# Kernel tuning notes

Measured on AMD Instinct MI355X. Metric: run time of the kernel, lower is better.

## Reference

```python
import jax, jax.numpy as jnp
import numpy as np

SCALES = [1, 2, 4]
DM = 768          # d_model
DS = 256          # d_scale = d_model / num_scales
DI = 512          # d_inner = expand * d_scale
N = 16            # d_state
K = 4             # d_conv (mamba causal conv)
R = 16            # dt_rank = ceil(d_scale/16)
B = 8
L = 1024
BN_EPS = 1e-5


def setup_inputs() -> dict:
    key = jax.random.key(0)
    ks = iter(jax.random.split(key, 64))
    def rn(shape, s=0.02):
        return jax.random.normal(next(ks), shape, jnp.float32) * s
    lengths = jax.random.randint(next(ks), (B,), L // 2, L + 1)
    mask = (jnp.arange(L)[None, :] < lengths[:, None]).astype(jnp.int32)
    return {
        "hidden_input": jax.random.normal(next(ks), (B, L, DM), jnp.float32),
        "mask": mask,
        # per-scale depthwise dilated conv + BN (eval-mode stats)
        "pool_w": rn((3, DS, 1, 3), 0.2),
        "pool_b": rn((3, DS)),
        "bn_g": jnp.ones((3, DS), jnp.float32),
        "bn_b": jnp.zeros((3, DS), jnp.float32),
        "bn_rm": jnp.zeros((3, DS), jnp.float32),
        "bn_rv": jnp.ones((3, DS), jnp.float32),
        # mamba params, axes = [scale(3), direction(2: fwd/bwd), ...]
        "in_proj_w": rn((3, 2, 2 * DI, DS)),
        "conv_w": rn((3, 2, DI, 1, K), 0.2),
        "conv_b": rn((3, 2, DI)),
        "x_proj_w": rn((3, 2, R + 2 * N, DI)),
        "dt_w": rn((3, 2, DI, R), 0.1),
        "dt_b": rn((3, 2, DI), 0.1),
        "A_log": jnp.broadcast_to(
            jnp.log(jnp.arange(1, N + 1, dtype=jnp.float32)), (3, 2, DI, N)
        ),
        "Dp": jnp.ones((3, 2, DI), jnp.float32),
        "mo_w": rn((3, 2, DS, DI)),
        # ExBimamba output_proj (2*d_scale -> d_scale, with bias)
        "op_w": rn((3, DS, 2 * DS)),
        "op_b": rn((3, DS)),
        # channel attention MLP (no bias) and fusion linear
        "ca_w1": rn((DM // 2, DM)),
        "ca_w2": rn((DM, DM // 2)),
        "fus_w": rn((DM, DM)),
        "fus_b": rn((DM,)),
    }


def _causal_dw_conv(x, w, b):
    # x: [B,L,D], w: [D,1,K] -> causal depthwise conv (left pad K-1)
    y = jax.lax.conv_general_dilated(
        x.transpose(0, 2, 1), w, (1,), [(K - 1, 0)],
        feature_group_count=w.shape[0], dimension_numbers=("NCH", "OIH", "NCH"))
    return y.transpose(0, 2, 1) + b


def _dilated_same_conv(x, w, b, dil):
    # x: [B,C,L], w: [C,1,3], depthwise, padding='same' with dilation
    y = jax.lax.conv_general_dilated(
        x, w, (1,), "SAME", rhs_dilation=(dil,),
        feature_group_count=x.shape[1], dimension_numbers=("NCH", "OIH", "NCH"))
    return y + b[:, None]


def _selective_scan(x, dt, A, Bm, Cm):
    # x, dt: [B,L,DI]; A: [DI,N]; Bm, Cm: [B,L,N]
    def step(h, inp):
        xt, dtt, Bt, Ct = inp
        h = h * jnp.exp(dtt[..., None] * A) + (dtt * xt)[..., None] * Bt[:, None, :]
        return h, jnp.einsum("bdn,bn->bd", h, Ct)
    h0 = jnp.zeros((x.shape[0], x.shape[2], A.shape[1]), x.dtype)
    _, ys = jax.lax.scan(
        step, h0,
        (x.swapaxes(0, 1), dt.swapaxes(0, 1), Bm.swapaxes(0, 1), Cm.swapaxes(0, 1)))
    return ys.swapaxes(0, 1)


def _mamba(u, iw, cw, cb, xw, dw, db, alog, D, ow):
    # u: [B,L,DS] -> [B,L,DS]
    x, z = jnp.split(u @ iw.T, 2, axis=-1)          # each [B,L,DI]
    x = jax.nn.silu(_causal_dw_conv(x, cw, cb))
    xdbl = x @ xw.T                                  # [B,L,R+2N]
    dt = jax.nn.softplus(xdbl[..., :R] @ dw.T + db)  # [B,L,DI]
    Bm, Cm = xdbl[..., R:R + N], xdbl[..., R + N:]
    y = _selective_scan(x, dt, -jnp.exp(alog), Bm, Cm) + x * D
    return (y * jax.nn.silu(z)) @ ow.T


def _mask_flip(x, lengths):
    # reverse the valid prefix of each row, keep padding in place (involution)
    j = jnp.arange(x.shape[1])
    idx = jnp.where(j[None, :] < lengths[:, None],
                    lengths[:, None] - 1 - j[None, :], j[None, :])
    return jnp.take_along_axis(x, idx[:, :, None], axis=1)


def reference(hidden_input, mask, pool_w, pool_b, bn_g, bn_b, bn_rm, bn_rv,
              in_proj_w, conv_w, conv_b, x_proj_w, dt_w, dt_b, A_log, Dp,
              mo_w, op_w, op_b, ca_w1, ca_w2, fus_w, fus_b):
    lengths = mask.sum(1)
    xs = jnp.split(hidden_input, 3, axis=-1)
    outs = []
    for i, s in enumerate(SCALES):
        c = _dilated_same_conv(xs[i].transpose(0, 2, 1), pool_w[i], pool_b[i], s)
        c = (c - bn_rm[i][:, None]) / jnp.sqrt(bn_rv[i][:, None] + BN_EPS) \
            * bn_g[i][:, None] + bn_b[i][:, None]
        c = jax.nn.gelu(c, approximate=False).transpose(0, 2, 1)  # [B,L,DS]
        f = _mamba(c, in_proj_w[i, 0], conv_w[i, 0], conv_b[i, 0], x_proj_w[i, 0],
                   dt_w[i, 0], dt_b[i, 0], A_log[i, 0], Dp[i, 0], mo_w[i, 0])
        bi = _mask_flip(c, lengths)
        bwd = _mamba(bi, in_proj_w[i, 1], conv_w[i, 1], conv_b[i, 1], x_proj_w[i, 1],
                     dt_w[i, 1], dt_b[i, 1], A_log[i, 1], Dp[i, 1], mo_w[i, 1])
        bwd = _mask_flip(bwd, lengths)
        outs.append(jnp.concatenate([f, bwd], -1) @ op_w[i].T + op_b[i])
    out = jnp.concatenate(outs, -1)                 # [B,L,DM]
    # channel attention: pools over the sequence (length) axis
    avg, mx = out.mean(1), out.max(1)
    def mlp(v):
        return jax.nn.relu(v @ ca_w1.T) @ ca_w2.T
    att = jax.nn.sigmoid(mlp(avg) + mlp(mx))
    out = out * att[:, None, :]
    return out @ fus_w.T + fus_b                    # dropout: eval-mode identity
```

## Files before the change

kernel.cpp:

```cpp
#include <hip/hip_runtime.h>
#include <cstddef>
#include <cstdint>

#define LQ 1024
#define DMQ 768
#define DSQ 256
#define DIQ 512
#define CCH 8
#define CT (LQ / CCH)

typedef unsigned short ushortT;
using f32x4 = __attribute__((ext_vector_type(4))) float;
using bf16x8 = __attribute__((ext_vector_type(8))) short;
using u16x8 = __attribute__((ext_vector_type(8))) unsigned short;

__device__ __forceinline__ float sigf(float x) { return 1.f / (1.f + __expf(-x)); }
__device__ __forceinline__ float softplusf(float x) {
    return fmaxf(x, 0.f) + __logf(1.f + __expf(-fabsf(x)));
}
__device__ __forceinline__ ushortT f2bf(float f) {
    unsigned u = __float_as_uint(f);
    u += 0x7FFFu + ((u >> 16) & 1u);
    return (ushortT)(u >> 16);
}
__device__ __forceinline__ float bf2f(ushortT u) {
    return __uint_as_float(((unsigned)u) << 16);
}
__device__ __forceinline__ void gload_lds16(const void* g, void* l) {
    __builtin_amdgcn_global_load_lds((const __attribute__((address_space(1))) void*)g,
                                     (__attribute__((address_space(3))) void*)l, 16, 0, 0);
}

__global__ void k_lengths(const int* __restrict__ mask, int* __restrict__ lengths) {
    int b = blockIdx.x;
    int s = 0;
    for (int t = threadIdx.x; t < LQ; t += 256) s += mask[b * LQ + t];
    __shared__ int sm[256];
    sm[threadIdx.x] = s;
    __syncthreads();
    for (int o = 128; o > 0; o >>= 1) {
        if (threadIdx.x < o) sm[threadIdx.x] += sm[threadIdx.x + o];
        __syncthreads();
    }
    if (threadIdx.x == 0) lengths[b] = sm[0];
}

__global__ void k_prep(const float* __restrict__ ipw, const float* __restrict__ fusw,
                       const float* __restrict__ xpw, ushortT* __restrict__ ipwb,
                       ushortT* __restrict__ fuswb, ushortT* __restrict__ xpwb) {
    int i = blockIdx.x * 256 + threadIdx.x;
    if (i < 1572864) { ipwb[i] = f2bf(ipw[i]); return; }
    i -= 1572864;
    if (i < 589824) { fuswb[i] = f2bf(fusw[i]); return; }
    i -= 589824;
    if (i >= 393216) return;
    int inst = i >> 16, rem = i & 65535;
    int row = rem >> 9, col = rem & 511;
    float v = (row < 48) ? xpw[((size_t)inst * 48 + row) * 512 + col] : 0.f;
    xpwb[i] = f2bf(v);
}

__global__ void k_wfuse(const float* __restrict__ opw, const float* __restrict__ mow,
                        ushortT* __restrict__ wf) {
    int idx = blockIdx.x * 256 + threadIdx.x;
    int inst = idx >> 15;
    int rem = idx & 32767;
    int m = rem >> 7;
    int d0 = (rem & 127) * 4;
    int i = inst >> 1, dir = inst & 1;
    const float* a = opw + (size_t)i * 131072 + dir * 256 + (size_t)m * 512;
    const float* bm = mow + (size_t)inst * 131072 + d0;
    float s0 = 0.f, s1 = 0.f, s2 = 0.f, s3 = 0.f;
    for (int c = 0; c < 256; c++) {
        float av = a[c];
        float4 bv = *(const float4*)(bm + (size_t)c * 512);
        s0 = fmaf(av, bv.x, s0);
        s1 = fmaf(av, bv.y, s1);
        s2 = fmaf(av, bv.z, s2);
        s3 = fmaf(av, bv.w, s3);
    }
    ushort4 r = {f2bf(s0), f2bf(s1), f2bf(s2), f2bf(s3)};
    *(ushort4*)(wf + ((size_t)i * 256 + m) * 1024 + dir * 512 + d0) = r;
}

__global__ void k_fusw8(const float* __restrict__ fusw, const float* __restrict__ att,
                        ushortT* __restrict__ wf8) {
    int idx = blockIdx.x * 256 + threadIdx.x;
    int b = idx / 147456;
    int rem = idx % 147456;
    int n = rem / 192;
    int k0 = (rem % 192) * 4;
    float4 w = *(const float4*)(fusw + (size_t)n * 768 + k0);
    float4 a = *(const float4*)(att + (size_t)b * 768 + k0);
    ushort4 r = {f2bf(w.x * a.x), f2bf(w.y * a.y), f2bf(w.z * a.z), f2bf(w.w * a.w)};
    *(ushort4*)(wf8 + ((size_t)(b * 768 + n)) * 768 + k0) = r;
}

__global__ __launch_bounds__(64) void k_pool(const float* __restrict__ hid,
                                             const float* __restrict__ pw,
                                             const float* __restrict__ pb,
                                             const float* __restrict__ bg,
                                             const float* __restrict__ bb,
                                             const float* __restrict__ brm,
                                             const float* __restrict__ brv,
                                             ushortT* __restrict__ cdst) {
    int gidx = blockIdx.x;
    int isc = gidx >> 13;
    int idx = gidx & 8191;
    int l = idx & (LQ - 1);
    int b = idx >> 10;
    int ch0 = threadIdx.x * 4;
    int dil = 1 << isc;
    int wci0 = isc * DSQ + ch0;
    const float* xb = hid + (size_t)b * LQ * DMQ + isc * DSQ + ch0;
    float wv[12];
    *(float4*)&wv[0] = *(const float4*)(pw + (size_t)wci0 * 3);
    *(float4*)&wv[4] = *(const float4*)(pw + (size_t)wci0 * 3 + 4);
    *(float4*)&wv[8] = *(const float4*)(pw + (size_t)wci0 * 3 + 8);
    float pbv[4], bgv[4], bbv[4], rmv[4], rvv[4];
    *(float4*)pbv = *(const float4*)(pb + wci0);
    *(float4*)bgv = *(const float4*)(bg + wci0);
    *(float4*)bbv = *(const float4*)(bb + wci0);
    *(float4*)rmv = *(const float4*)(brm + wci0);
    *(float4*)rvv = *(const float4*)(brv + wci0);
    float xm[4] = {0.f, 0.f, 0.f, 0.f}, xc[4], xp[4] = {0.f, 0.f, 0.f, 0.f};
    int lm = l - dil, lp = l + dil;
    if (lm >= 0) *(float4*)xm = *(const float4*)(xb + (size_t)lm * DMQ);
    *(float4*)xc = *(const float4*)(xb + (size_t)l * DMQ);
    if (lp < LQ) *(float4*)xp = *(const float4*)(xb + (size_t)lp * DMQ);
    ushort4 o;
#pragma unroll
    for (int j = 0; j < 4; j++) {
        float acc = pbv[j];
        acc = fmaf(wv[j * 3 + 0], xm[j], acc);
        acc = fmaf(wv[j * 3 + 1], xc[j], acc);
        acc = fmaf(wv[j * 3 + 2], xp[j], acc);
        float xn = (acc - rmv[j]) * rsqrtf(rvv[j] + 1e-5f) * bgv[j] + bbv[j];
        float y = 0.5f * xn * (1.0f + erff(xn * 0.70710678118654752f));
        ((ushortT*)&o)[j] = f2bf(y);
    }
    *(ushort4*)(cdst + (size_t)isc * 2097152 + (size_t)idx * DSQ + ch0) = o;
}

template <int FLIPA, int FLIPC, int BIAS, int ACC, int CBF16, int GATE>
__global__ __launch_bounds__(256) void gemm_bf16(
    const ushortT* __restrict__ A, const ushortT* __restrict__ Bw, void* __restrict__ Cv,
    const float* __restrict__ bias, const ushortT* __restrict__ Yb,
    const int* __restrict__ lengths, int N, int Kd, int lda, int ldc, int ldy, long sAz,
    int zshiftA, long sBz, long sCz, long sCzOdd, int zshiftC, long sYz, int sBiasz) {
    __shared__ ushortT Als[128 * 64];
    __shared__ ushortT Bls[128 * 64];
    const int z = blockIdx.z;
    A += (size_t)(z >> zshiftA) * sAz;
    Bw += (size_t)z * sBz;
    size_t cbase = (size_t)(z >> zshiftC) * sCz +
                   (size_t)(z & ((1 << zshiftC) - 1)) * sCzOdd;
    float* Cf = (float*)Cv + (CBF16 ? 0 : cbase);
    ushortT* Cb = (ushortT*)Cv + (CBF16 ? cbase : 0);
    if (BIAS) bias += (size_t)z * sBiasz;
    if (GATE) Yb += (size_t)z * sYz;

    const int tid = threadIdx.x;
    const int lane = tid & 63;
    const int wave = tid >> 6;
    const int wr = wave >> 1, wc = wave & 1;
    const int row0 = blockIdx.y * 128, col0 = blockIdx.x * 128;
    const bool doflipA = (FLIPA == 1) || (FLIPA == 2 && (z & 1));
    const bool doflipC = (FLIPC == 1) || (FLIPC == 2 && (z & 1));
    int len = 0;
    if (FLIPA || FLIPC) len = lengths[row0 >> 10];

    const int srow = wave * 8 + (lane >> 3);
    const int scol = (lane & 7) * 8;

    f32x4 acc[4][4];
#pragma unroll
    for (int i = 0; i < 4; i++)
#pragma unroll
        for (int j = 0; j < 4; j++) acc[i][j] = (f32x4){0.f, 0.f, 0.f, 0.f};

    for (int k0 = 0; k0 < Kd; k0 += 64) {
        __syncthreads();
#pragma unroll
        for (int it = 0; it < 4; it++) {
            int row = it * 32 + srow;
            int grow = row0 + row;
            if (FLIPA) {
                if (doflipA) {
                    int t = grow & (LQ - 1);
                    int ts = (t < len) ? (len - 1 - t) : t;
                    grow = (grow & ~(LQ - 1)) | ts;
                }
            }
            gload_lds16(A + (size_t)grow * lda + k0 + scol, &Als[it * 2048 + wave * 512]);
        }
#pragma unroll
        for (int it = 0; it < 4; it++) {
            int row = it * 32 + srow;
            gload_lds16(Bw + (size_t)(col0 + row) * Kd + k0 + scol,
                        &Bls[it * 2048 + wave * 512]);
        }
        __syncthreads();
#pragma unroll
        for (int ks = 0; ks < 2; ks++) {
            bf16x8 am[4], bv[4];
#pragma unroll
            for (int f = 0; f < 4; f++) {
                am[f] = *(const bf16x8*)&Als[(wr * 64 + f * 16 + (lane & 15)) * 64 + ks * 32 +
                                             (lane >> 4) * 8];
                bv[f] = *(const bf16x8*)&Bls[(wc * 64 + f * 16 + (lane & 15)) * 64 + ks * 32 +
                                             (lane >> 4) * 8];
            }
#pragma unroll
            for (int fm = 0; fm < 4; fm++)
#pragma unroll
                for (int fn = 0; fn < 4; fn++)
                    acc[fm][fn] = __builtin_amdgcn_mfma_f32_16x16x32_bf16(am[fm], bv[fn],
                                                                          acc[fm][fn], 0, 0, 0);
        }
    }
#pragma unroll
    for (int fm = 0; fm < 4; fm++) {
#pragma unroll
        for (int r = 0; r < 4; r++) {
            int growY = row0 + wr * 64 + fm * 16 + (lane >> 4) * 4 + r;
            int growC = growY;
            if (FLIPC) {
                if (doflipC) {
                    int t = growC & (LQ - 1);
                    int ts = (t < len) ? (len - 1 - t) : t;
                    growC = (growC & ~(LQ - 1)) | ts;
                }
            }
#pragma unroll
            for (int fn = 0; fn < 4; fn++) {
                int col = col0 + wc * 64 + fn * 16 + (lane & 15);
                if (col < N) {
                    float v = acc[fm][fn][r];
                    if (CBF16) {
                        if (GATE) {
                            float yv = bf2f(Yb[(size_t)growY * ldy + col]);
                            v = yv * v * sigf(v);
                        }
                        if (BIAS) v += bias[col];
                        Cb[(size_t)growC * ldc + col] = f2bf(v);
                    } else {
                        float* cp = Cf + (size_t)growC * ldc + col;
                        if (ACC) v += *cp;
                        if (BIAS) v += bias[col];
                        *cp = v;
                    }
                }
            }
        }
    }
}

__global__ __launch_bounds__(256) void k_dwconv(const ushortT* __restrict__ rawx,
                                                const float* __restrict__ cw,
                                                const float* __restrict__ cb,
                                                ushortT* __restrict__ sx) {
    int blk = blockIdx.x;
    int tc = blk & 7;
    int sb = blk >> 3;
    int inst = sb >> 3;
    int cg = threadIdx.x & 63;
    int sub = threadIdx.x >> 6;
    int ch0 = cg * 8;
    int t0 = tc * 128 + sub * 32;
    const ushortT* base = rawx + (size_t)sb * LQ * DIQ + ch0;
    ushortT* obase = sx + (size_t)sb * LQ * DIQ + ch0;

    float w[8][4], bs[8];
#pragma unroll
    for (int j = 0; j < 8; j++) {
        float4 wv = *(const float4*)(cw + (size_t)inst * 2048 + (size_t)(ch0 + j) * 4);
        w[j][0] = wv.x; w[j][1] = wv.y; w[j][2] = wv.z; w[j][3] = wv.w;
        bs[j] = cb[inst * DIQ + ch0 + j];
    }
    float x3[8], x2[8], x1[8];
#pragma unroll
    for (int j = 0; j < 8; j++) { x3[j] = 0.f; x2[j] = 0.f; x1[j] = 0.f; }
    if (t0 >= 3) {
        u16x8 v3 = *(const u16x8*)(base + (size_t)(t0 - 3) * DIQ);
        u16x8 v2 = *(const u16x8*)(base + (size_t)(t0 - 2) * DIQ);
        u16x8 v1 = *(const u16x8*)(base + (size_t)(t0 - 1) * DIQ);
#pragma unroll
        for (int j = 0; j < 8; j++) {
            x3[j] = bf2f(v3[j]); x2[j] = bf2f(v2[j]); x1[j] = bf2f(v1[j]);
        }
    }
#pragma unroll 4
    for (int t = t0; t < t0 + 32; t++) {
        u16x8 v = *(const u16x8*)(base + (size_t)t * DIQ);
        float xc[8];
#pragma unroll
        for (int j = 0; j < 8; j++) xc[j] = bf2f(v[j]);
        u16x8 o;
#pragma unroll
        for (int j = 0; j < 8; j++) {
            float acc = bs[j];
            acc = fmaf(w[j][0], x3[j], acc);
            acc = fmaf(w[j][1], x2[j], acc);
            acc = fmaf(w[j][2], x1[j], acc);
            acc = fmaf(w[j][3], xc[j], acc);
            o[j] = f2bf(acc * sigf(acc));
        }
        *(u16x8*)(obase + (size_t)t * DIQ) = o;
#pragma unroll
        for (int j = 0; j < 8; j++) { x3[j] = x2[j]; x2[j] = x1[j]; x1[j] = xc[j]; }
    }
}

__global__ __launch_bounds__(256) void k_scan1(ushortT* __restrict__ scanX,
                                               const float* __restrict__ xdbl,
                                               const float* __restrict__ dt_w,
                                               const float* __restrict__ dt_b,
                                               const float* __restrict__ A_log,
                                               const float* __restrict__ Dpp,
                                               float* __restrict__ hbuf,
                                               float* __restrict__ sbuf) {
    int bid = blockIdx.x;
    int seq = bid >> 4;
    int r = bid & 15;
    int c = r >> 1, half = r & 1;
    int inst = seq >> 3;
    int ch = half * 256 + threadIdx.x;

    const float4* xd4 = (const float4*)(xdbl + ((size_t)seq * LQ + c * CT) * 48);
    ushortT* xp = scanX + ((size_t)seq * LQ + c * CT) * DIQ + ch;
    int wo = inst * DIQ + ch;
    float dtw[16], Ad[16];
#pragma unroll
    for (int rr = 0; rr < 16; rr++) dtw[rr] = dt_w[(size_t)wo * 16 + rr];
    float dtb = dt_b[wo];
    bool fastA = true;
#pragma unroll
    for (int n = 0; n < 16; n++) {
        Ad[n] = -__expf(A_log[(size_t)wo * 16 + n]);
        fastA = fastA && (fabsf(Ad[n] + (float)(n + 1)) < 1e-3f * (n + 1));
    }
    float Dd = Dpp[wo];
    float h[16];
#pragma unroll
    for (int n = 0; n < 16; n++) h[n] = 0.f;
    float S = 0.f;

    __shared__ float4 sd4[CT * 12];
    for (int u = threadIdx.x; u < CT * 12; u += 256) sd4[u] = xd4[u];
    __syncthreads();

    float xt = bf2f(xp[0]);
    if (fastA) {
        for (int tl = 0; tl < CT; tl++) {
            float xnext = (tl + 1 < CT) ? bf2f(xp[(size_t)(tl + 1) * DIQ]) : 0.f;
            const float4* s4 = sd4 + tl * 12;
            float4 q0 = s4[0], q1 = s4[1], q2 = s4[2], q3 = s4[3];
            float draw = dtb;
            draw = fmaf(q0.x, dtw[0], draw); draw = fmaf(q0.y, dtw[1], draw);
            draw = fmaf(q0.z, dtw[2], draw); draw = fmaf(q0.w, dtw[3], draw);
            draw = fmaf(q1.x, dtw[4], draw); draw = fmaf(q1.y, dtw[5], draw);
            draw = fmaf(q1.z, dtw[6], draw); draw = fmaf(q1.w, dtw[7], draw);
            draw = fmaf(q2.x, dtw[8], draw); draw = fmaf(q2.y, dtw[9], draw);
            draw = fmaf(q2.z, dtw[10], draw); draw = fmaf(q2.w, dtw[11], draw);
            draw = fmaf(q3.x, dtw[12], draw); draw = fmaf(q3.y, dtw[13], draw);
            draw = fmaf(q3.z, dtw[14], draw); draw = fmaf(q3.w, dtw[15], draw);
            float dt = softplusf(draw);
            S += dt;
            float e1 = __expf(-dt);
            float dtx = dt * xt;
            float bb[16], cc[16];
            *(float4*)&bb[0] = s4[4]; *(float4*)&bb[4] = s4[5];
            *(float4*)&bb[8] = s4[6]; *(float4*)&bb[12] = s4[7];
            *(float4*)&cc[0] = s4[8]; *(float4*)&cc[4] = s4[9];
            *(float4*)&cc[8] = s4[10]; *(float4*)&cc[12] = s4[11];
            float y = 0.f, e = 1.f;
#pragma unroll
            for (int n = 0; n < 16; n++) {
                e *= e1;
                h[n] = fmaf(h[n], e, dtx * bb[n]);
                y = fmaf(h[n], cc[n], y);
            }
            xp[(size_t)tl * DIQ] = f2bf(fmaf(xt, Dd, y));
            xt = xnext;
        }
    } else {
        for (int tl = 0; tl < CT; tl++) {
            float xnext = (tl + 1 < CT) ? bf2f(xp[(size_t)(tl + 1) * DIQ]) : 0.f;
            const float4* s4 = sd4 + tl * 12;
            float qq[16], bb[16], cc[16];
            *(float4*)&qq[0] = s4[0]; *(float4*)&qq[4] = s4[1];
            *(float4*)&qq[8] = s4[2]; *(float4*)&qq[12] = s4[3];
            *(float4*)&bb[0] = s4[4]; *(float4*)&bb[4] = s4[5];
            *(float4*)&bb[8] = s4[6]; *(float4*)&bb[12] = s4[7];
            *(float4*)&cc[0] = s4[8]; *(float4*)&cc[4] = s4[9];
            *(float4*)&cc[8] = s4[10]; *(float4*)&cc[12] = s4[11];
            float draw = dtb;
#pragma unroll
            for (int rr = 0; rr < 16; rr++) draw = fmaf(qq[rr], dtw[rr], draw);
            float dt = softplusf(draw);
            S += dt;
            float dtx = dt * xt;
            float y = 0.f;
#pragma unroll
            for (int n = 0; n < 16; n++) {
                float e = __expf(dt * Ad[n]);
                h[n] = fmaf(h[n], e, dtx * bb[n]);
                y = fmaf(h[n], cc[n], y);
            }
            xp[(size_t)tl * DIQ] = f2bf(fmaf(xt, Dd, y));
            xt = xnext;
        }
    }
    size_t hb = ((size_t)(seq * CCH + c) * 16) * DIQ + ch;
#pragma unroll
    for (int n = 0; n < 16; n++) hbuf[hb + (size_t)n * DIQ] = h[n];
    sbuf[(size_t)(seq * CCH + c) * DIQ + ch] = S;
}

__global__ __launch_bounds__(512) void k_scan2(const float* __restrict__ A_log,
                                               float* __restrict__ hbuf,
                                               const float* __restrict__ sbuf) {
    int seq = blockIdx.x;
    int inst = seq >> 3;
    int ch = threadIdx.x;
    int wo = inst * DIQ + ch;
    float Ad[16];
#pragma unroll
    for (int n = 0; n < 16; n++) Ad[n] = -__expf(A_log[(size_t)wo * 16 + n]);
    float hin[16];
#pragma unroll
    for (int n = 0; n < 16; n++) hin[n] = 0.f;
    for (int c = 0; c < CCH; c++) {
        size_t hb = ((size_t)(seq * CCH + c) * 16) * DIQ + ch;
        float Sc = sbuf[(size_t)(seq * CCH + c) * DIQ + ch];
        float he[16];
#pragma unroll
        for (int n = 0; n < 16; n++) he[n] = hbuf[hb + (size_t)n * DIQ];
#pragma unroll
        for (int n = 0; n < 16; n++) hbuf[hb + (size_t)n * DIQ] = hin[n];
#pragma unroll
        for (int n = 0; n < 16; n++) hin[n] = fmaf(hin[n], __expf(Ad[n] * Sc), he[n]);
    }
}

__global__ __launch_bounds__(256) void k_scan3(ushortT* __restrict__ scanX,
                                               const float* __restrict__ xdbl,
                                               const float* __restrict__ dt_w,
                                               const float* __restrict__ dt_b,
                                               const float* __restrict__ A_log,
                                               const float* __restrict__ hbuf) {
    int bid = blockIdx.x;
    int seq = bid / (2 * (CCH - 1));
    int r = bid % (2 * (CCH - 1));
    int c = 1 + (r >> 1), half = r & 1;
    int inst = seq >> 3;
    int ch = half * 256 + threadIdx.x;

    const float4* xd4 = (const float4*)(xdbl + ((size_t)seq * LQ + c * CT) * 48);
    ushortT* xp = scanX + ((size_t)seq * LQ + c * CT) * DIQ + ch;
    int wo = inst * DIQ + ch;
    float dtw[16], Ad[16];
#pragma unroll
    for (int rr = 0; rr < 16; rr++) dtw[rr] = dt_w[(size_t)wo * 16 + rr];
    float dtb = dt_b[wo];
    float amax = -1e30f;
    bool fastA = true;
#pragma unroll
    for (int n = 0; n < 16; n++) {
        Ad[n] = -__expf(A_log[(size_t)wo * 16 + n]);
        amax = fmaxf(amax, Ad[n]);
        fastA = fastA && (fabsf(Ad[n] + (float)(n + 1)) < 1e-3f * (n + 1));
    }
    float hin[16];
    size_t hb = ((size_t)(seq * CCH + c) * 16) * DIQ + ch;
#pragma unroll
    for (int n = 0; n < 16; n++) hin[n] = hbuf[hb + (size_t)n * DIQ];

    __shared__ float4 sd4[CT * 12];
    for (int u = threadIdx.x; u < CT * 12; u += 256) sd4[u] = xd4[u];
    __syncthreads();

    float S = 0.f;
    for (int tl = 0; tl < CT; tl++) {
        const float4* s4 = sd4 + tl * 12;
        float4 q0 = s4[0], q1 = s4[1], q2 = s4[2], q3 = s4[3];
        float draw = dtb;
        draw = fmaf(q0.x, dtw[0], draw); draw = fmaf(q0.y, dtw[1], draw);
        draw = fmaf(q0.z, dtw[2], draw); draw = fmaf(q0.w, dtw[3], draw);
        draw = fmaf(q1.x, dtw[4], draw); draw = fmaf(q1.y, dtw[5], draw);
        draw = fmaf(q1.z, dtw[6], draw); draw = fmaf(q1.w, dtw[7], draw);
        draw = fmaf(q2.x, dtw[8], draw); draw = fmaf(q2.y, dtw[9], draw);
        draw = fmaf(q2.z, dtw[10], draw); draw = fmaf(q2.w, dtw[11], draw);
        draw = fmaf(q3.x, dtw[12], draw); draw = fmaf(q3.y, dtw[13], draw);
        draw = fmaf(q3.z, dtw[14], draw); draw = fmaf(q3.w, dtw[15], draw);
        S += softplusf(draw);
        if (__all(amax * S < -30.f)) break;
        float cc[16];
        *(float4*)&cc[0] = s4[8]; *(float4*)&cc[4] = s4[9];
        *(float4*)&cc[8] = s4[10]; *(float4*)&cc[12] = s4[11];
        float corr = 0.f;
        if (fastA) {
            float eS = __expf(-S);
            float e = 1.f;
#pragma unroll
            for (int n = 0; n < 16; n++) {
                e *= eS;
                corr = fmaf(e * hin[n], cc[n], corr);
            }
        } else {
#pragma unroll
            for (int n = 0; n < 16; n++)
                corr = fmaf(__expf(Ad[n] * S) * hin[n], cc[n], corr);
        }
        xp[(size_t)tl * DIQ] = f2bf(bf2f(xp[(size_t)tl * DIQ]) + corr);
    }
}

__global__ void k_redu1(const ushortT* __restrict__ mo, float* __restrict__ psum,
                        float* __restrict__ pmax) {
    int b = blockIdx.x >> 5, tc = blockIdx.x & 31;
    int ch0 = threadIdx.x * 4;
    const ushortT* p = mo + ((size_t)b * LQ + tc * 32) * DMQ + ch0;
    float s[4] = {0.f, 0.f, 0.f, 0.f};
    float m[4] = {-3.4e38f, -3.4e38f, -3.4e38f, -3.4e38f};
    for (int t = 0; t < 32; t++) {
        ushort4 v = *(const ushort4*)(p + (size_t)t * DMQ);
        float f0 = bf2f(v.x), f1 = bf2f(v.y), f2 = bf2f(v.z), f3 = bf2f(v.w);
        s[0] += f0; s[1] += f1; s[2] += f2; s[3] += f3;
        m[0] = fmaxf(m[0], f0); m[1] = fmaxf(m[1], f1);
        m[2] = fmaxf(m[2], f2); m[3] = fmaxf(m[3], f3);
    }
    *(float4*)(psum + (size_t)(b * 32 + tc) * DMQ + ch0) = *(float4*)s;
    *(float4*)(pmax + (size_t)(b * 32 + tc) * DMQ + ch0) = *(float4*)m;
}

__global__ void k_redu2(const float* __restrict__ psum, const float* __restrict__ pmax,
                        float* __restrict__ avg, float* __restrict__ mx) {
    int idx = blockIdx.x * 256 + threadIdx.x;
    int b = idx / DMQ, ch = idx % DMQ;
    float s = 0.f, m = -3.4e38f;
    for (int tc = 0; tc < 32; tc++) {
        s += psum[(size_t)(b * 32 + tc) * DMQ + ch];
        m = fmaxf(m, pmax[(size_t)(b * 32 + tc) * DMQ + ch]);
    }
    avg[idx] = s * (1.f / LQ);
    mx[idx] = m;
}

__global__ __launch_bounds__(256) void k_att1(const float* __restrict__ avg,
                                              const float* __restrict__ mx,
                                              const float* __restrict__ w1,
                                              float* __restrict__ hs) {
    int gw = (blockIdx.x * 256 + threadIdx.x) >> 6;
    int lane = threadIdx.x & 63;
    int b = gw / 384, j = gw % 384;
    const float* w = w1 + (size_t)j * DMQ;
    const float* a = avg + (size_t)b * DMQ;
    const float* m2 = mx + (size_t)b * DMQ;
    float s1 = 0.f, s2 = 0.f;
#pragma unroll
    for (int it = 0; it < 3; it++) {
        int k = it * 256 + lane * 4;
        float4 wv = *(const float4*)(w + k);
        float4 av = *(const float4*)(a + k);
        float4 mv = *(const float4*)(m2 + k);
        s1 = fmaf(av.x, wv.x, s1); s1 = fmaf(av.y, wv.y, s1);
        s1 = fmaf(av.z, wv.z, s1); s1 = fmaf(av.w, wv.w, s1);
        s2 = fmaf(mv.x, wv.x, s2); s2 = fmaf(mv.y, wv.y, s2);
        s2 = fmaf(mv.z, wv.z, s2); s2 = fmaf(mv.w, wv.w, s2);
    }
#pragma unroll
    for (int o = 32; o > 0; o >>= 1) {
        s1 += __shfl_xor(s1, o);
        s2 += __shfl_xor(s2, o);
    }
    if (lane == 0) hs[gw] = fmaxf(s1, 0.f) + fmaxf(s2, 0.f);
}

__global__ __launch_bounds__(256) void k_att2(const float* __restrict__ hs,
                                              const float* __restrict__ w2,
                                              float* __restrict__ att) {
    int gw = (blockIdx.x * 256 + threadIdx.x) >> 6;
    int lane = threadIdx.x & 63;
    int b = gw / DMQ, n = gw % DMQ;
    const float* w = w2 + (size_t)n * 384;
    const float* h = hs + (size_t)b * 384;
    float s = 0.f;
#pragma unroll
    for (int it = 0; it < 3; it++) {
        int k = it * 128 + lane * 2;
        float2 wv = *(const float2*)(w + k);
        float2 hv = *(const float2*)(h + k);
        s = fmaf(hv.x, wv.x, s);
        s = fmaf(hv.y, wv.y, s);
    }
#pragma unroll
    for (int o = 32; o > 0; o >>= 1) s += __shfl_xor(s, o);
    if (lane == 0) att[gw] = sigf(s);
}

__global__ void k_diag(float* __restrict__ o, float v) {
    if (blockIdx.x == 0 && threadIdx.x == 0) o[0] = v;
}

extern "C" void kernel_launch(void* const* d_in, const int* in_sizes, int n_in, void* d_out,
                              int out_size, void* d_ws, size_t ws_size, hipStream_t stream) {
    (void)in_sizes; (void)n_in; (void)out_size;
    const float* hid = (const float*)d_in[0];
    const int* mask = (const int*)d_in[1];
    const float* pool_w = (const float*)d_in[2];
    const float* pool_b = (const float*)d_in[3];
    const float* bn_g = (const float*)d_in[4];
    const float* bn_b = (const float*)d_in[5];
    const float* bn_rm = (const float*)d_in[6];
    const float* bn_rv = (const float*)d_in[7];
    const float* ipw = (const float*)d_in[8];
    const float* cw = (const float*)d_in[9];
    const float* cb = (const float*)d_in[10];
    const float* xpw = (const float*)d_in[11];
    const float* dtw = (const float*)d_in[12];
    const float* dtb = (const float*)d_in[13];
    const float* alog = (const float*)d_in[14];
    const float* Dpp = (const float*)d_in[15];
    const float* mow = (const float*)d_in[16];
    const float* opw = (const float*)d_in[17];
    const float* opb = (const float*)d_in[18];
    const float* caw1 = (const float*)d_in[19];
    const float* caw2 = (const float*)d_in[20];
    const float* fusw = (const float*)d_in[21];
    const float* fusb = (const float*)d_in[22];
    float* out = (float*)d_out;

    const size_t O_IPWB = 32768;
    const size_t O_XPWB = 819200;
    const size_t O_FUSWB = 1015808;
    const size_t O_WTMPB = 1310720;
    const size_t O_XDBL = 1703936;
    const size_t O_CBASE = 4063232;
    const size_t O_RAWX = 7208960;
    const size_t O_SCANX = 19791872;
    const size_t TOTAL_F = 32374784;
    if (ws_size < TOTAL_F * 4) {
        k_diag<<<1, 64, 0, stream>>>(out, (float)(ws_size >> 20));
        return;
    }

    float* ws = (float*)d_ws;
    int* lengths = (int*)ws;
    float* att = ws + 1024;
    float* avg = att + 6144;
    float* mxp = avg + 6144;
    float* hs = mxp + 6144;
    ushortT* ipwb = (ushortT*)(ws + O_IPWB);
    ushortT* xpwb = (ushortT*)(ws + O_XPWB);
    ushortT* fuswb = (ushortT*)(ws + O_FUSWB);
    ushortT* wtmpb = (ushortT*)(ws + O_WTMPB);
    float* xdbl = ws + O_XDBL;
    ushortT* cbase = (ushortT*)(ws + O_CBASE);
    ushortT* rawx = (ushortT*)(ws + O_RAWX);
    ushortT* scanX = (ushortT*)(ws + O_SCANX);
    float* hbuf = ws + O_RAWX;
    float* sbuf = hbuf + 3145728;
    ushortT* gbuf = rawx;
    ushortT* moutb = cbase;
    float* psum = ws + O_SCANX;
    float* pmax = psum + 196608;
    ushortT* fuswb8 = (ushortT*)(pmax + 196608);

    k_lengths<<<dim3(8), dim3(256), 0, stream>>>(mask, lengths);
    k_prep<<<dim3(9984), dim3(256), 0, stream>>>(ipw, fusw, xpw, ipwb, fuswb, xpwb);
    k_wfuse<<<dim3(768), dim3(256), 0, stream>>>(opw, mow, wtmpb);

    k_pool<<<dim3(3 * 8192), dim3(64), 0, stream>>>(hid, pool_w, pool_b, bn_g, bn_b, bn_rm,
                                                    bn_rv, cbase);

    gemm_bf16<2, 0, 0, 0, 1, 0><<<dim3(4, 64, 6), 256, 0, stream>>>(
        cbase, ipwb, rawx, nullptr, nullptr, lengths, 512, 256, 256, 512, 0, 2097152, 1,
        262144, 4194304, 0, 0, 0, 0);

    k_dwconv<<<dim3(384), dim3(256), 0, stream>>>(rawx, cw, cb, scanX);

    gemm_bf16<0, 0, 0, 0, 0, 0><<<dim3(1, 64, 6), 256, 0, stream>>>(
        scanX, xpwb, xdbl, nullptr, nullptr, lengths, 48, 512, 512, 48, 0, 4194304, 0, 65536,
        393216, 0, 0, 0, 0);

    k_scan1<<<dim3(48 * CCH * 2), dim3(256), 0, stream>>>(scanX, xdbl, dtw, dtb, alog, Dpp,
                                                          hbuf, sbuf);
    k_scan2<<<dim3(48), dim3(512), 0, stream>>>(alog, hbuf, sbuf);
    k_scan3<<<dim3(48 * (CCH - 1) * 2), dim3(256), 0, stream>>>(scanX, xdbl, dtw, dtb, alog,
                                                                hbuf);

    gemm_bf16<2, 2, 0, 0, 1, 1><<<dim3(4, 64, 6), 256, 0, stream>>>(
        cbase, ipwb + 131072, gbuf, nullptr, scanX, lengths, 512, 256, 256, 1024, 512,
        2097152, 1, 262144, 8388608, 512, 1, 4194304, 0);

    gemm_bf16<0, 0, 1, 0, 1, 0><<<dim3(2, 64, 3), 256, 0, stream>>>(
        gbuf, wtmpb, moutb, opb, nullptr, lengths, 256, 1024, 1024, 768, 0, 8388608, 0,
        262144, 256, 0, 0, 0, 256);

    k_redu1<<<dim3(256), dim3(192), 0, stream>>>(moutb, psum, pmax);
    k_redu2<<<dim3(24), dim3(256), 0, stream>>>(psum, pmax, avg, mxp);
    k_att1<<<dim3(768), dim3(256), 0, stream>>>(avg, mxp, caw1, hs);
    k_att2<<<dim3(1536), dim3(256), 0, stream>>>(hs, caw2, att);
    k_fusw8<<<dim3(4608), dim3(256), 0, stream>>>(fusw, att, fuswb8);
    gemm_bf16<0, 0, 1, 0, 0, 0><<<dim3(6, 8, 8), 256, 0, stream>>>(
        moutb, fuswb8, out, fusb, nullptr, lengths, DMQ, DMQ, DMQ, DMQ, 0, 786432, 0, 589824,
        786432, 0, 0, 0, 0);
}
```

Measured before the change: 418.2 us.

## Precompute dt softplus once in separate kernel, shared by both scan passes

```diff
diff --git a/kernel.cpp b/kernel.cpp
--- a/kernel.cpp
+++ b/kernel.cpp
@@ -45,14 +45,11 @@
     if (threadIdx.x == 0) lengths[b] = sm[0];
 }
 
-__global__ void k_prep(const float* __restrict__ ipw, const float* __restrict__ fusw,
-                       const float* __restrict__ xpw, ushortT* __restrict__ ipwb,
-                       ushortT* __restrict__ fuswb, ushortT* __restrict__ xpwb) {
+__global__ void k_prep(const float* __restrict__ ipw, const float* __restrict__ xpw,
+                       ushortT* __restrict__ ipwb, ushortT* __restrict__ xpwb) {
     int i = blockIdx.x * 256 + threadIdx.x;
     if (i < 1572864) { ipwb[i] = f2bf(ipw[i]); return; }
     i -= 1572864;
-    if (i < 589824) { fuswb[i] = f2bf(fusw[i]); return; }
-    i -= 589824;
     if (i >= 393216) return;
     int inst = i >> 16, rem = i & 65535;
     int row = rem >> 9, col = rem & 511;
@@ -96,20 +93,22 @@
     *(ushort4*)(wf8 + ((size_t)(b * 768 + n)) * 768 + k0) = r;
 }
 
-__global__ __launch_bounds__(64) void k_pool(const float* __restrict__ hid,
-                                             const float* __restrict__ pw,
-                                             const float* __restrict__ pb,
-                                             const float* __restrict__ bg,
-                                             const float* __restrict__ bb,
-                                             const float* __restrict__ brm,
-                                             const float* __restrict__ brv,
-                                             ushortT* __restrict__ cdst) {
+__global__ __launch_bounds__(256) void k_pool(const float* __restrict__ hid,
+                                              const float* __restrict__ pw,
+                                              const float* __restrict__ pb,
+                                              const float* __restrict__ bg,
+                                              const float* __restrict__ bb,
+                                              const float* __restrict__ brm,
+                                              const float* __restrict__ brv,
+                                              ushortT* __restrict__ cdst) {
     int gidx = blockIdx.x;
-    int isc = gidx >> 13;
-    int idx = gidx & 8191;
-    int l = idx & (LQ - 1);
-    int b = idx >> 10;
-    int ch0 = threadIdx.x * 4;
+    int isc = gidx / 2048;
+    int rem = gidx % 2048;
+    int b = rem >> 8;
+    int lgrp = rem & 255;
+    int l = lgrp * 4 + (threadIdx.x >> 6);
+    int idx = b * LQ + l;
+    int ch0 = (threadIdx.x & 63) * 4;
     int dil = 1 << isc;
     int wci0 = isc * DSQ + ch0;
     const float* xb = hid + (size_t)b * LQ * DMQ + isc * DSQ + ch0;
@@ -312,10 +311,48 @@
     }
 }
 
+__global__ __launch_bounds__(256) void k_dt(const float* __restrict__ xdbl,
+                                            const float* __restrict__ dt_w,
+                                            const float* __restrict__ dt_b,
+                                            ushortT* __restrict__ dtb16) {
+    int bid = blockIdx.x;
+    int seq = bid >> 4, tc = bid & 15;
+    int inst = seq >> 3;
+    int ch0 = threadIdx.x * 2;
+    const float4* xd4 = (const float4*)(xdbl + ((size_t)seq * LQ + tc * 64) * 48);
+    __shared__ float4 sd4[64 * 4];
+    for (int u = threadIdx.x; u < 64 * 4; u += 256) {
+        int t = u >> 2, q = u & 3;
+        sd4[u] = xd4[t * 12 + q];
+    }
+    __syncthreads();
+    float w0[16], w1[16];
+    const float4* wp = (const float4*)(dt_w + ((size_t)inst * 512 + ch0) * 16);
+    *(float4*)&w0[0] = wp[0]; *(float4*)&w0[4] = wp[1];
+    *(float4*)&w0[8] = wp[2]; *(float4*)&w0[12] = wp[3];
+    *(float4*)&w1[0] = wp[4]; *(float4*)&w1[4] = wp[5];
+    *(float4*)&w1[8] = wp[6]; *(float4*)&w1[12] = wp[7];
+    float b0 = dt_b[inst * 512 + ch0], b1 = dt_b[inst * 512 + ch0 + 1];
+    ushortT* op = dtb16 + ((size_t)seq * LQ + tc * 64) * DIQ + ch0;
+    for (int t = 0; t < 64; t++) {
+        const float4* s4 = sd4 + t * 4;
+        float q[16];
+        *(float4*)&q[0] = s4[0]; *(float4*)&q[4] = s4[1];
+        *(float4*)&q[8] = s4[2]; *(float4*)&q[12] = s4[3];
+        float d0 = b0, d1 = b1;
+#pragma unroll
+        for (int r = 0; r < 16; r++) {
+            d0 = fmaf(q[r], w0[r], d0);
+            d1 = fmaf(q[r], w1[r], d1);
+        }
+        ushort2 o = {f2bf(softplusf(d0)), f2bf(softplusf(d1))};
+        *(ushort2*)(op + (size_t)t * DIQ) = o;
+    }
+}
+
 __global__ __launch_bounds__(256) void k_scan1(ushortT* __restrict__ scanX,
                                                const float* __restrict__ xdbl,
-                                               const float* __restrict__ dt_w,
-                                               const float* __restrict__ dt_b,
+                                               const ushortT* __restrict__ dtb16,
                                                const float* __restrict__ A_log,
                                                const float* __restrict__ Dpp,
                                                float* __restrict__ hbuf,
@@ -329,11 +366,9 @@
 
     const float4* xd4 = (const float4*)(xdbl + ((size_t)seq * LQ + c * CT) * 48);
     ushortT* xp = scanX + ((size_t)seq * LQ + c * CT) * DIQ + ch;
+    const ushortT* dtp = dtb16 + ((size_t)seq * LQ + c * CT) * DIQ + ch;
     int wo = inst * DIQ + ch;
-    float dtw[16], Ad[16];
-#pragma unroll
-    for (int rr = 0; rr < 16; rr++) dtw[rr] = dt_w[(size_t)wo * 16 + rr];
-    float dtb = dt_b[wo];
+    float Ad[16];
     bool fastA = true;
 #pragma unroll
     for (int n = 0; n < 16; n++) {
@@ -346,34 +381,29 @@
     for (int n = 0; n < 16; n++) h[n] = 0.f;
     float S = 0.f;
 
-    __shared__ float4 sd4[CT * 12];
-    for (int u = threadIdx.x; u < CT * 12; u += 256) sd4[u] = xd4[u];
+    __shared__ float4 sd4[CT * 8];
+    for (int u = threadIdx.x; u < CT * 8; u += 256) {
+        int t = u >> 3, q = u & 7;
+        sd4[u] = xd4[t * 12 + 4 + q];
+    }
     __syncthreads();
 
     float xt = bf2f(xp[0]);
+    float dtc = bf2f(dtp[0]);
     if (fastA) {
         for (int tl = 0; tl < CT; tl++) {
             float xnext = (tl + 1 < CT) ? bf2f(xp[(size_t)(tl + 1) * DIQ]) : 0.f;
-            const float4* s4 = sd4 + tl * 12;
-            float4 q0 = s4[0], q1 = s4[1], q2 = s4[2], q3 = s4[3];
-            float draw = dtb;
-            draw = fmaf(q0.x, dtw[0], draw); draw = fmaf(q0.y, dtw[1], draw);
-            draw = fmaf(q0.z, dtw[2], draw); draw = fmaf(q0.w, dtw[3], draw);
-            draw = fmaf(q1.x, dtw[4], draw); draw = fmaf(q1.y, dtw[5], draw);
-            draw = fmaf(q1.z, dtw[6], draw); draw = fmaf(q1.w, dtw[7], draw);
-            draw = fmaf(q2.x, dtw[8], draw); draw = fmaf(q2.y, dtw[9], draw);
-            draw = fmaf(q2.z, dtw[10], draw); draw = fmaf(q2.w, dtw[11], draw);
-            draw = fmaf(q3.x, dtw[12], draw); draw = fmaf(q3.y, dtw[13], draw);
-            draw = fmaf(q3.z, dtw[14], draw); draw = fmaf(q3.w, dtw[15], draw);
-            float dt = softplusf(draw);
+            float dtn = (tl + 1 < CT) ? bf2f(dtp[(size_t)(tl + 1) * DIQ]) : 0.f;
+            const float4* s4 = sd4 + tl * 8;
+            float dt = dtc;
             S += dt;
             float e1 = __expf(-dt);
             float dtx = dt * xt;
             float bb[16], cc[16];
-            *(float4*)&bb[0] = s4[4]; *(float4*)&bb[4] = s4[5];
-            *(float4*)&bb[8] = s4[6]; *(float4*)&bb[12] = s4[7];
-            *(float4*)&cc[0] = s4[8]; *(float4*)&cc[4] = s4[9];
-            *(float4*)&cc[8] = s4[10]; *(float4*)&cc[12] = s4[11];
+            *(float4*)&bb[0] = s4[0]; *(float4*)&bb[4] = s4[1];
+            *(float4*)&bb[8] = s4[2]; *(float4*)&bb[12] = s4[3];
+            *(float4*)&cc[0] = s4[4]; *(float4*)&cc[4] = s4[5];
+            *(float4*)&cc[8] = s4[6]; *(float4*)&cc[12] = s4[7];
             float y = 0.f, e = 1.f;
 #pragma unroll
             for (int n = 0; n < 16; n++) {
@@ -383,24 +413,21 @@
             }
             xp[(size_t)tl * DIQ] = f2bf(fmaf(xt, Dd, y));
             xt = xnext;
+            dtc = dtn;
         }
     } else {
         for (int tl = 0; tl < CT; tl++) {
             float xnext = (tl + 1 < CT) ? bf2f(xp[(size_t)(tl + 1) * DIQ]) : 0.f;
-            const float4* s4 = sd4 + tl * 12;
-            float qq[16], bb[16], cc[16];
-            *(float4*)&qq[0] = s4[0]; *(float4*)&qq[4] = s4[1];
-            *(float4*)&qq[8] = s4[2]; *(float4*)&qq[12] = s4[3];
-            *(float4*)&bb[0] = s4[4]; *(float4*)&bb[4] = s4[5];
-            *(float4*)&bb[8] = s4[6]; *(float4*)&bb[12] = s4[7];
-            *(float4*)&cc[0] = s4[8]; *(float4*)&cc[4] = s4[9];
-            *(float4*)&cc[8] = s4[10]; *(float4*)&cc[12] = s4[11];
-            float draw = dtb;
-#pragma unroll
-            for (int rr = 0; rr < 16; rr++) draw = fmaf(qq[rr], dtw[rr], draw);
-            float dt = softplusf(draw);
+            float dtn = (tl + 1 < CT) ? bf2f(dtp[(size_t)(tl + 1) * DIQ]) : 0.f;
+            const float4* s4 = sd4 + tl * 8;
+            float dt = dtc;
             S += dt;
             float dtx = dt * xt;
+            float bb[16], cc[16];
+            *(float4*)&bb[0] = s4[0]; *(float4*)&bb[4] = s4[1];
+            *(float4*)&bb[8] = s4[2]; *(float4*)&bb[12] = s4[3];
+            *(float4*)&cc[0] = s4[4]; *(float4*)&cc[4] = s4[5];
+            *(float4*)&cc[8] = s4[6]; *(float4*)&cc[12] = s4[7];
             float y = 0.f;
 #pragma unroll
             for (int n = 0; n < 16; n++) {
@@ -410,6 +437,7 @@
             }
             xp[(size_t)tl * DIQ] = f2bf(fmaf(xt, Dd, y));
             xt = xnext;
+            dtc = dtn;
         }
     }
     size_t hb = ((size_t)(seq * CCH + c) * 16) * DIQ + ch;
@@ -446,8 +474,7 @@
 
 __global__ __launch_bounds__(256) void k_scan3(ushortT* __restrict__ scanX,
                                                const float* __restrict__ xdbl,
-                                               const float* __restrict__ dt_w,
-                                               const float* __restrict__ dt_b,
+                                               const ushortT* __restrict__ dtb16,
                                                const float* __restrict__ A_log,
                                                const float* __restrict__ hbuf) {
     int bid = blockIdx.x;
@@ -459,11 +486,9 @@
 
     const float4* xd4 = (const float4*)(xdbl + ((size_t)seq * LQ + c * CT) * 48);
     ushortT* xp = scanX + ((size_t)seq * LQ + c * CT) * DIQ + ch;
+    const ushortT* dtp = dtb16 + ((size_t)seq * LQ + c * CT) * DIQ + ch;
     int wo = inst * DIQ + ch;
-    float dtw[16], Ad[16];
-#pragma unroll
-    for (int rr = 0; rr < 16; rr++) dtw[rr] = dt_w[(size_t)wo * 16 + rr];
-    float dtb = dt_b[wo];
+    float Ad[16];
     float amax = -1e30f;
     bool fastA = true;
 #pragma unroll
@@ -477,28 +502,21 @@
 #pragma unroll
     for (int n = 0; n < 16; n++) hin[n] = hbuf[hb + (size_t)n * DIQ];
 
-    __shared__ float4 sd4[CT * 12];
-    for (int u = threadIdx.x; u < CT * 12; u += 256) sd4[u] = xd4[u];
+    __shared__ float4 sd4[CT * 4];
+    for (int u = threadIdx.x; u < CT * 4; u += 256) {
+        int t = u >> 2, q = u & 3;
+        sd4[u] = xd4[t * 12 + 8 + q];
+    }
     __syncthreads();
 
     float S = 0.f;
     for (int tl = 0; tl < CT; tl++) {
-        const float4* s4 = sd4 + tl * 12;
-        float4 q0 = s4[0], q1 = s4[1], q2 = s4[2], q3 = s4[3];
-        float draw = dtb;
-        draw = fmaf(q0.x, dtw[0], draw); draw = fmaf(q0.y, dtw[1], draw);
-        draw = fmaf(q0.z, dtw[2], draw); draw = fmaf(q0.w, dtw[3], draw);
-        draw = fmaf(q1.x, dtw[4], draw); draw = fmaf(q1.y, dtw[5], draw);
-        draw = fmaf(q1.z, dtw[6], draw); draw = fmaf(q1.w, dtw[7], draw);
-        draw = fmaf(q2.x, dtw[8], draw); draw = fmaf(q2.y, dtw[9], draw);
-        draw = fmaf(q2.z, dtw[10], draw); draw = fmaf(q2.w, dtw[11], draw);
-        draw = fmaf(q3.x, dtw[12], draw); draw = fmaf(q3.y, dtw[13], draw);
-        draw = fmaf(q3.z, dtw[14], draw); draw = fmaf(q3.w, dtw[15], draw);
-        S += softplusf(draw);
+        S += bf2f(dtp[(size_t)tl * DIQ]);
         if (__all(amax * S < -30.f)) break;
+        const float4* s4 = sd4 + tl * 4;
         float cc[16];
-        *(float4*)&cc[0] = s4[8]; *(float4*)&cc[4] = s4[9];
-        *(float4*)&cc[8] = s4[10]; *(float4*)&cc[12] = s4[11];
+        *(float4*)&cc[0] = s4[0]; *(float4*)&cc[4] = s4[1];
+        *(float4*)&cc[8] = s4[2]; *(float4*)&cc[12] = s4[3];
         float corr = 0.f;
         if (fastA) {
             float eS = __expf(-S);
@@ -634,13 +652,13 @@
 
     const size_t O_IPWB = 32768;
     const size_t O_XPWB = 819200;
-    const size_t O_FUSWB = 1015808;
     const size_t O_WTMPB = 1310720;
     const size_t O_XDBL = 1703936;
     const size_t O_CBASE = 4063232;
     const size_t O_RAWX = 7208960;
     const size_t O_SCANX = 19791872;
-    const size_t TOTAL_F = 32374784;
+    const size_t O_HBUF = 32374784;
+    const size_t TOTAL_F = 35717120;
     if (ws_size < TOTAL_F * 4) {
         k_diag<<<1, 64, 0, stream>>>(out, (float)(ws_size >> 20));
         return;
@@ -654,14 +672,14 @@
     float* hs = mxp + 6144;
     ushortT* ipwb = (ushortT*)(ws + O_IPWB);
     ushortT* xpwb = (ushortT*)(ws + O_XPWB);
-    ushortT* fuswb = (ushortT*)(ws + O_FUSWB);
     ushortT* wtmpb = (ushortT*)(ws + O_WTMPB);
     float* xdbl = ws + O_XDBL;
     ushortT* cbase = (ushortT*)(ws + O_CBASE);
     ushortT* rawx = (ushortT*)(ws + O_RAWX);
     ushortT* scanX = (ushortT*)(ws + O_SCANX);
-    float* hbuf = ws + O_RAWX;
+    float* hbuf = ws + O_HBUF;
     float* sbuf = hbuf + 3145728;
+    ushortT* dtb16 = rawx;
     ushortT* gbuf = rawx;
     ushortT* moutb = cbase;
     float* psum = ws + O_SCANX;
@@ -669,11 +687,11 @@
     ushortT* fuswb8 = (ushortT*)(pmax + 196608);
 
     k_lengths<<<dim3(8), dim3(256), 0, stream>>>(mask, lengths);
-    k_prep<<<dim3(9984), dim3(256), 0, stream>>>(ipw, fusw, xpw, ipwb, fuswb, xpwb);
+    k_prep<<<dim3(7680), dim3(256), 0, stream>>>(ipw, xpw, ipwb, xpwb);
     k_wfuse<<<dim3(768), dim3(256), 0, stream>>>(opw, mow, wtmpb);
 
-    k_pool<<<dim3(3 * 8192), dim3(64), 0, stream>>>(hid, pool_w, pool_b, bn_g, bn_b, bn_rm,
-                                                    bn_rv, cbase);
+    k_pool<<<dim3(6144), dim3(256), 0, stream>>>(hid, pool_w, pool_b, bn_g, bn_b, bn_rm,
+                                                 bn_rv, cbase);
 
     gemm_bf16<2, 0, 0, 0, 1, 0><<<dim3(4, 64, 6), 256, 0, stream>>>(
         cbase, ipwb, rawx, nullptr, nullptr, lengths, 512, 256, 256, 512, 0, 2097152, 1,
@@ -685,10 +703,12 @@
         scanX, xpwb, xdbl, nullptr, nullptr, lengths, 48, 512, 512, 48, 0, 4194304, 0, 65536,
         393216, 0, 0, 0, 0);
 
-    k_scan1<<<dim3(48 * CCH * 2), dim3(256), 0, stream>>>(scanX, xdbl, dtw, dtb, alog, Dpp,
-                                                          hbuf, sbuf);
+    k_dt<<<dim3(48 * 16), dim3(256), 0, stream>>>(xdbl, dtw, dtb, dtb16);
+
+    k_scan1<<<dim3(48 * CCH * 2), dim3(256), 0, stream>>>(scanX, xdbl, dtb16, alog, Dpp, hbuf,
+                                                          sbuf);
     k_scan2<<<dim3(48), dim3(512), 0, stream>>>(alog, hbuf, sbuf);
-    k_scan3<<<dim3(48 * (CCH - 1) * 2), dim3(256), 0, stream>>>(scanX, xdbl, dtw, dtb, alog,
+    k_scan3<<<dim3(48 * (CCH - 1) * 2), dim3(256), 0, stream>>>(scanX, xdbl, dtb16, alog,
                                                                 hbuf);
 
     gemm_bf16<2, 2, 0, 0, 1, 1><<<dim3(4, 64, 6), 256, 0, stream>>>(
```

Result: slower. 438.5 us (+4.8%).
